# Kernel tuning notes

Hardware: AMD Instinct MI355X
Metric: run time of the kernel (lower is better)

Reference implementation:

```python
import jax, jax.numpy as jnp
import numpy as np

N = 2          # batch (upsample scale for sample i is i+1, shapes chosen so no crop occurs)
C = 512        # channels for both branches
TH = TW = 256  # target H,W taken from pts_feats[0]
IMG_SIZES = [128, 64, 32, 16, 8]  # 5-level FPN
BN_EPS = 1e-5


def setup_inputs() -> dict:
    key = jax.random.key(0)
    ks = jax.random.split(key, 24)
    inp = {}
    for l, s in enumerate(IMG_SIZES):
        inp[f'img_feat{l}'] = jax.random.normal(ks[l], (N, C, s, s), jnp.float32)
    inp['pts_feat0'] = jax.random.normal(ks[5], (N, C, TH, TW), jnp.float32)
    # 1x1 conv + BN params (eval-mode BN with running stats)
    inp['img_w'] = jax.random.normal(ks[6], (C, C), jnp.float32) * 0.02
    inp['img_b'] = jax.random.normal(ks[7], (C,), jnp.float32) * 0.02
    inp['img_gamma'] = jnp.ones((C,), jnp.float32)
    inp['img_beta'] = jnp.zeros((C,), jnp.float32)
    inp['img_mean'] = jnp.zeros((C,), jnp.float32)
    inp['img_var'] = jax.random.uniform(ks[8], (C,), jnp.float32, 0.5, 1.5)
    inp['pts_w'] = jax.random.normal(ks[9], (C, C), jnp.float32) * 0.02
    inp['pts_b'] = jax.random.normal(ks[10], (C,), jnp.float32) * 0.02
    inp['pts_gamma'] = jnp.ones((C,), jnp.float32)
    inp['pts_beta'] = jnp.zeros((C,), jnp.float32)
    inp['pts_mean'] = jnp.zeros((C,), jnp.float32)
    inp['pts_var'] = jax.random.uniform(ks[11], (C,), jnp.float32, 0.5, 1.5)
    return inp


def _obtain_mlvl(feats, th, tw):
    # Faithful to original: per-sample loop (scale_factor depends on batch index,
    # so each sample has a different static upsampled shape -> Python loop over N=2).
    n = feats[0].shape[0]
    outs = []
    for i in range(n):
        acc = None
        for lvl, f in enumerate(feats):
            x = f[i]  # [C, h, w]
            if lvl > 0:
                s = i + 1  # nearest upsample by batch-index+1 (as in source)
                x = jnp.repeat(jnp.repeat(x, s, axis=1), s, axis=2)
            dh = th - x.shape[1]
            dw = tw - x.shape[2]
            x = jnp.pad(x, ((0, 0), (dh // 2, dh - dh // 2), (dw // 2, dw - dw // 2)), mode='edge')
            acc = x if acc is None else acc + x
        outs.append(acc)
    return jnp.stack(outs, 0)  # [N, C, th, tw]


def _conv_bn_relu(x, w, b, gamma, beta, mean, var):
    # 1x1 conv == channel contraction, then eval-mode BN, then ReLU
    y = jnp.einsum('nchw,oc->nohw', x, w) + b[None, :, None, None]
    scale = gamma / jnp.sqrt(var + BN_EPS)
    y = (y - mean[None, :, None, None]) * scale[None, :, None, None] + beta[None, :, None, None]
    return jax.nn.relu(y)


def reference(img_feat0, img_feat1, img_feat2, img_feat3, img_feat4, pts_feat0,
              img_w, img_b, img_gamma, img_beta, img_mean, img_var,
              pts_w, pts_b, pts_gamma, pts_beta, pts_mean, pts_var):
    th, tw = pts_feat0.shape[2], pts_feat0.shape[3]
    pts_m = _obtain_mlvl([pts_feat0], th, tw)  # pts_levels=1
    pts_pre = _conv_bn_relu(pts_m, pts_w, pts_b, pts_gamma, pts_beta, pts_mean, pts_var)
    img_m = _obtain_mlvl([img_feat0, img_feat1, img_feat2, img_feat3, img_feat4], th, tw)
    img_pre = _conv_bn_relu(img_m, img_w, img_b, img_gamma, img_beta, img_mean, img_var)
    # dropout is identity in eval mode (deterministic reference)
    return jnp.concatenate((img_pre, pts_pre), axis=1)  # [N, 2C, th, tw]
```

## Files before the change

### kernel.cpp

```cpp
#include <hip/hip_runtime.h>

typedef unsigned short u16;
typedef __attribute__((ext_vector_type(8))) short s8frag;
typedef __attribute__((ext_vector_type(4))) float f32x4;

#define GLOAD16(gp, lp)                                                        \
  __builtin_amdgcn_global_load_lds(                                            \
      (const __attribute__((address_space(1))) void*)(gp),                     \
      (__attribute__((address_space(3))) void*)(lp), 16, 0, 0)

__device__ __forceinline__ u16 f2bf(float x) {
  unsigned int u = __float_as_uint(x);
  unsigned int r = (u + 0x7fffu + ((u >> 16) & 1u)) >> 16;
  return (u16)r;
}

__global__ __launch_bounds__(256) void prep_w(
    const float* __restrict__ wi, const float* __restrict__ bi,
    const float* __restrict__ gi, const float* __restrict__ bei,
    const float* __restrict__ mi, const float* __restrict__ vi,
    const float* __restrict__ wp, const float* __restrict__ bp,
    const float* __restrict__ gp, const float* __restrict__ bep,
    const float* __restrict__ mp, const float* __restrict__ vp,
    u16* __restrict__ wout_i, float* __restrict__ bias_i,
    u16* __restrict__ wout_p, float* __restrict__ bias_p) {
  int gidx = blockIdx.x * 256 + threadIdx.x;
  int branch = gidx >> 18;
  int idx = gidx & ((1 << 18) - 1);
  int o = idx >> 9, c = idx & 511;
  const float* w = branch ? wp : wi;
  const float* b = branch ? bp : bi;
  const float* g = branch ? gp : gi;
  const float* be = branch ? bep : bei;
  const float* mn = branch ? mp : mi;
  const float* vr = branch ? vp : vi;
  u16* wo = branch ? wout_p : wout_i;
  float* bo = branch ? bias_p : bias_i;
  float scale = g[o] * rsqrtf(vr[o] + 1e-5f);
  wo[idx] = f2bf(w[idx] * scale);
  if (c == 0) bo[o] = scale * (b[o] - mn[o]) + be[o];
}

__global__ __launch_bounds__(256) void build_b(
    const float* __restrict__ f0, const float* __restrict__ f1,
    const float* __restrict__ f2, const float* __restrict__ f3,
    const float* __restrict__ f4, const float* __restrict__ pts,
    u16* __restrict__ Bimg, u16* __restrict__ Bpts) {
  __shared__ float tile[64][65];
  int t = threadIdx.x;
  int wblk = blockIdx.x;
  int h = blockIdx.y;
  int z = blockIdx.z;
  bool is_img = z < 16;
  int zz = is_img ? z : z - 16;
  int n = zz >> 3;
  int cblk = zz & 7;
  int cbase = cblk * 64;

  if (is_img) {
    int wl = t & 63, w = wblk * 64 + wl;
    const float* feats[5] = {f0, f1, f2, f3, f4};
    const int S[5] = {128, 64, 32, 16, 8};
    int off[5];
#pragma unroll
    for (int l = 0; l < 5; ++l) {
      int s = S[l];
      int scale = (n == 1 && l > 0) ? 2 : 1;
      int u = s * scale, pad = (256 - u) >> 1;
      int ih = h - pad; ih = ih < 0 ? 0 : (ih > u - 1 ? u - 1 : ih); ih /= scale;
      int iw = w - pad; iw = iw < 0 ? 0 : (iw > u - 1 ? u - 1 : iw); iw /= scale;
      off[l] = ih * s + iw;
    }
    for (int cs = 0; cs < 16; ++cs) {
      int cl = cs * 4 + (t >> 6);
      int c = cbase + cl;
      float acc = 0.f;
#pragma unroll
      for (int l = 0; l < 5; ++l) {
        int s = S[l];
        acc += feats[l][(long)(n * 512 + c) * s * s + off[l]];
      }
      tile[cl][wl] = acc;
    }
  } else {
    int wq = t & 15;
    int cl0 = t >> 4;
#pragma unroll
    for (int j = 0; j < 4; ++j) {
      int cl = cl0 + j * 16;
      int c = cbase + cl;
      float4 v = *(const float4*)&pts[((long)(n * 512 + c) * 256 + h) * 256 +
                                      wblk * 64 + wq * 4];
      tile[cl][wq * 4 + 0] = v.x;
      tile[cl][wq * 4 + 1] = v.y;
      tile[cl][wq * 4 + 2] = v.z;
      tile[cl][wq * 4 + 3] = v.w;
    }
  }
  __syncthreads();

  u16* dst = is_img ? Bimg : Bpts;
  long hwb = (long)h * 256 + wblk * 64;
#pragma unroll
  for (int half = 0; half < 2; ++half) {
    int c0 = (t & 7) * 8;
    int wl2 = half * 32 + (t >> 3);
    u16 p[8];
#pragma unroll
    for (int j = 0; j < 8; ++j) p[j] = f2bf(tile[c0 + j][wl2]);
    long di = ((long)n * 65536 + hwb + wl2) * 512 + cbase + c0;
    *(uint4*)(dst + di) = *(const uint4*)p;
  }
}

__global__ __launch_bounds__(256) void gemm_fused(
    const u16* __restrict__ Aimg, const u16* __restrict__ Apts,
    const u16* __restrict__ Bimg, const u16* __restrict__ Bpts,
    const float* __restrict__ biasImg, const float* __restrict__ biasPts,
    float* __restrict__ out) {
  int br = blockIdx.z;
  const u16* A = br ? Apts : Aimg;
  const u16* B = br ? Bpts : Bimg;
  const float* bias = br ? biasPts : biasImg;

  int s = blockIdx.x;
  int w = (s & 7) * 512 + (s >> 3);
  int rt = w & 3;
  int ct = w >> 2;
  int n = ct >> 9;
  int colbase = (ct & 511) * 128;
  const u16* Bn = B + ((long)n * 65536) * 512;

  __shared__ u16 As[3][128 * 32];
  __shared__ u16 Bs[3][128 * 32];

  int t = threadIdx.x;
  int wave = t >> 6, lane = t & 63;
  int wr = wave >> 1, wc = wave & 1;
  int lrow = lane & 15;
  int q = lane >> 4;

  f32x4 acc[4][4] = {};

#define STAGE_A(buf, kk)                                                      \
  {                                                                           \
    _Pragma("unroll") for (int i = 0; i < 2; ++i) {                           \
      int slot = t + i * 256;                                                 \
      int row = slot >> 2, kp = slot & 3;                                     \
      int sw = (row >> 1) & 3;                                                \
      GLOAD16(A + ((long)(rt * 128 + row) * 512 + (kk) + ((kp ^ sw) * 8)),    \
              &As[buf][slot * 8]);                                            \
    }                                                                         \
  }
#define STAGE_B(buf, kk)                                                      \
  {                                                                           \
    _Pragma("unroll") for (int i = 0; i < 2; ++i) {                           \
      int slot = t + i * 256;                                                 \
      int row = slot >> 2, kp = slot & 3;                                     \
      int sw = (row >> 1) & 3;                                                \
      GLOAD16(Bn + ((long)(colbase + row) * 512 + (kk) + ((kp ^ sw) * 8)),    \
              &Bs[buf][slot * 8]);                                            \
    }                                                                         \
  }

  STAGE_A(0, 0);
  STAGE_B(0, 0);
  STAGE_A(1, 32);
  STAGE_B(1, 32);
  asm volatile("s_waitcnt vmcnt(4)" ::: "memory");
  __builtin_amdgcn_s_barrier();

  for (int kt = 0; kt < 16; ++kt) {
    int cur = kt % 3;
    int nb = (kt + 2) % 3;
    s8frag a0, a1, b[4];
    {
      int r0 = wr * 64 + 0 * 16 + lrow;
      a0 = *(const s8frag*)&As[cur][r0 * 32 + ((q ^ ((r0 >> 1) & 3)) * 8)];
      int r1 = wr * 64 + 1 * 16 + lrow;
      a1 = *(const s8frag*)&As[cur][r1 * 32 + ((q ^ ((r1 >> 1) & 3)) * 8)];
#pragma unroll
      for (int nn = 0; nn < 4; ++nn) {
        int r = wc * 64 + nn * 16 + lrow;
        b[nn] = *(const s8frag*)&Bs[cur][r * 32 + ((q ^ ((r >> 1) & 3)) * 8)];
      }
    }
    if (kt < 14) STAGE_A(nb, (kt + 2) * 32);
    __builtin_amdgcn_s_setprio(1);
#pragma unroll
    for (int nn = 0; nn < 4; ++nn)
      acc[0][nn] = __builtin_amdgcn_mfma_f32_16x16x32_bf16(a0, b[nn], acc[0][nn], 0, 0, 0);
#pragma unroll
    for (int nn = 0; nn < 4; ++nn)
      acc[1][nn] = __builtin_amdgcn_mfma_f32_16x16x32_bf16(a1, b[nn], acc[1][nn], 0, 0, 0);
    __builtin_amdgcn_s_setprio(0);
    __builtin_amdgcn_s_barrier();

    s8frag a2, a3;
    {
      int r2 = wr * 64 + 2 * 16 + lrow;
      a2 = *(const s8frag*)&As[cur][r2 * 32 + ((q ^ ((r2 >> 1) & 3)) * 8)];
      int r3 = wr * 64 + 3 * 16 + lrow;
      a3 = *(const s8frag*)&As[cur][r3 * 32 + ((q ^ ((r3 >> 1) & 3)) * 8)];
    }
    if (kt < 14) STAGE_B(nb, (kt + 2) * 32);
    __builtin_amdgcn_s_setprio(1);
#pragma unroll
    for (int nn = 0; nn < 4; ++nn)
      acc[2][nn] = __builtin_amdgcn_mfma_f32_16x16x32_bf16(a2, b[nn], acc[2][nn], 0, 0, 0);
#pragma unroll
    for (int nn = 0; nn < 4; ++nn)
      acc[3][nn] = __builtin_amdgcn_mfma_f32_16x16x32_bf16(a3, b[nn], acc[3][nn], 0, 0, 0);
    __builtin_amdgcn_s_setprio(0);
    if (kt < 15) {
      if (kt < 14)
        asm volatile("s_waitcnt vmcnt(4)" ::: "memory");
      else
        asm volatile("s_waitcnt vmcnt(0)" ::: "memory");
      __builtin_amdgcn_s_barrier();
    }
  }
#undef STAGE_A
#undef STAGE_B

  long outbase = ((long)n * 1024 + br * 512) * 65536;
#pragma unroll
  for (int m = 0; m < 4; ++m) {
    int o0 = rt * 128 + wr * 64 + m * 16 + (lane >> 4) * 4;
#pragma unroll
    for (int nn = 0; nn < 4; ++nn) {
      int hw = colbase + wc * 64 + nn * 16 + (lane & 15);
#pragma unroll
      for (int j = 0; j < 4; ++j) {
        int o = o0 + j;
        float v = acc[m][nn][j] + bias[o];
        v = v > 0.f ? v : 0.f;
        out[outbase + (long)o * 65536 + hw] = v;
      }
    }
  }
}

extern "C" void kernel_launch(void* const* d_in, const int* in_sizes, int n_in,
                              void* d_out, int out_size, void* d_ws,
                              size_t ws_size, hipStream_t stream) {
  (void)in_sizes; (void)n_in; (void)out_size; (void)ws_size;
  const float* f0 = (const float*)d_in[0];
  const float* f1 = (const float*)d_in[1];
  const float* f2 = (const float*)d_in[2];
  const float* f3 = (const float*)d_in[3];
  const float* f4 = (const float*)d_in[4];
  const float* pts = (const float*)d_in[5];
  const float* img_w = (const float*)d_in[6];
  const float* img_b = (const float*)d_in[7];
  const float* img_gamma = (const float*)d_in[8];
  const float* img_beta = (const float*)d_in[9];
  const float* img_mean = (const float*)d_in[10];
  const float* img_var = (const float*)d_in[11];
  const float* pts_w = (const float*)d_in[12];
  const float* pts_b = (const float*)d_in[13];
  const float* pts_gamma = (const float*)d_in[14];
  const float* pts_beta = (const float*)d_in[15];
  const float* pts_mean = (const float*)d_in[16];
  const float* pts_var = (const float*)d_in[17];

  char* ws = (char*)d_ws;
  u16* wA_img = (u16*)ws;
  u16* wA_pts = wA_img + 512 * 512;
  float* bias_img = (float*)(ws + (1u << 20));
  float* bias_pts = bias_img + 512;
  u16* Bimg = (u16*)(ws + (2u << 20));
  u16* Bpts = Bimg + (size_t)2 * 65536 * 512;

  prep_w<<<2048, 256, 0, stream>>>(img_w, img_b, img_gamma, img_beta, img_mean,
                                   img_var, pts_w, pts_b, pts_gamma, pts_beta,
                                   pts_mean, pts_var, wA_img, bias_img, wA_pts,
                                   bias_pts);
  build_b<<<dim3(4, 256, 32), 256, 0, stream>>>(f0, f1, f2, f3, f4, pts, Bimg,
                                                Bpts);
  gemm_fused<<<dim3(4096, 1, 2), 256, 0, stream>>>(
      wA_img, wA_pts, Bimg, Bpts, bias_img, bias_pts, (float*)d_out);
}
```

Before: 485.1 us.

## Load GEMM fragments directly from global memory, dropping LDS staging and barriers

Replaces the triple-buffered LDS pipeline (global_load_lds plus swizzled LDS reads and barriers) with direct per-wave global loads of the MFMA operand fragments, register double-buffered across K steps. It also sets launch bounds to request three blocks per CU. The aim is to remove the LDS traffic and synchronisation overhead, at the cost of redundant global/L2 reads: each A and B fragment row is now fetched by two waves instead of once per block. The 16-byte per-lane loads stride 1 KB between rows, so coalescing is poorer than before.

```diff
diff --git a/kernel.cpp b/kernel.cpp
--- a/kernel.cpp
+++ b/kernel.cpp
@@ -3,11 +3,6 @@
 typedef unsigned short u16;
 typedef __attribute__((ext_vector_type(8))) short s8frag;
 typedef __attribute__((ext_vector_type(4))) float f32x4;
-
-#define GLOAD16(gp, lp)                                                        \
-  __builtin_amdgcn_global_load_lds(                                            \
-      (const __attribute__((address_space(1))) void*)(gp),                     \
-      (__attribute__((address_space(3))) void*)(lp), 16, 0, 0)
 
 __device__ __forceinline__ u16 f2bf(float x) {
   unsigned int u = __float_as_uint(x);
@@ -113,7 +108,7 @@
   }
 }
 
-__global__ __launch_bounds__(256) void gemm_fused(
+__global__ __launch_bounds__(256, 3) void gemm_direct(
     const u16* __restrict__ Aimg, const u16* __restrict__ Apts,
     const u16* __restrict__ Bimg, const u16* __restrict__ Bpts,
     const float* __restrict__ biasImg, const float* __restrict__ biasPts,
@@ -131,97 +126,46 @@
   int colbase = (ct & 511) * 128;
   const u16* Bn = B + ((long)n * 65536) * 512;
 
-  __shared__ u16 As[3][128 * 32];
-  __shared__ u16 Bs[3][128 * 32];
-
   int t = threadIdx.x;
   int wave = t >> 6, lane = t & 63;
   int wr = wave >> 1, wc = wave & 1;
   int lrow = lane & 15;
   int q = lane >> 4;
 
+  const u16* pa = A + ((long)(rt * 128 + wr * 64 + lrow) * 512) + q * 8;
+  const u16* pb = Bn + ((long)(colbase + wc * 64 + lrow) * 512) + q * 8;
+
   f32x4 acc[4][4] = {};
-
-#define STAGE_A(buf, kk)                                                      \
+  s8frag aX[4], bX[4], aY[4], bY[4];
+
+#define LOADF(av, bv, kt_)                                                    \
   {                                                                           \
-    _Pragma("unroll") for (int i = 0; i < 2; ++i) {                           \
-      int slot = t + i * 256;                                                 \
-      int row = slot >> 2, kp = slot & 3;                                     \
-      int sw = (row >> 1) & 3;                                                \
-      GLOAD16(A + ((long)(rt * 128 + row) * 512 + (kk) + ((kp ^ sw) * 8)),    \
-              &As[buf][slot * 8]);                                            \
-    }                                                                         \
-  }
-#define STAGE_B(buf, kk)                                                      \
+    _Pragma("unroll") for (int m = 0; m < 4; ++m)                             \
+        av[m] = *(const s8frag*)(pa + (long)m * 8192 + (kt_) * 32);           \
+    _Pragma("unroll") for (int nn = 0; nn < 4; ++nn)                          \
+        bv[nn] = *(const s8frag*)(pb + (long)nn * 8192 + (kt_) * 32);         \
+  }
+#define MF(av, bv)                                                            \
   {                                                                           \
-    _Pragma("unroll") for (int i = 0; i < 2; ++i) {                           \
-      int slot = t + i * 256;                                                 \
-      int row = slot >> 2, kp = slot & 3;                                     \
-      int sw = (row >> 1) & 3;                                                \
-      GLOAD16(Bn + ((long)(colbase + row) * 512 + (kk) + ((kp ^ sw) * 8)),    \
-              &Bs[buf][slot * 8]);                                            \
-    }                                                                         \
-  }
-
-  STAGE_A(0, 0);
-  STAGE_B(0, 0);
-  STAGE_A(1, 32);
-  STAGE_B(1, 32);
-  asm volatile("s_waitcnt vmcnt(4)" ::: "memory");
-  __builtin_amdgcn_s_barrier();
-
-  for (int kt = 0; kt < 16; ++kt) {
-    int cur = kt % 3;
-    int nb = (kt + 2) % 3;
-    s8frag a0, a1, b[4];
-    {
-      int r0 = wr * 64 + 0 * 16 + lrow;
-      a0 = *(const s8frag*)&As[cur][r0 * 32 + ((q ^ ((r0 >> 1) & 3)) * 8)];
-      int r1 = wr * 64 + 1 * 16 + lrow;
-      a1 = *(const s8frag*)&As[cur][r1 * 32 + ((q ^ ((r1 >> 1) & 3)) * 8)];
-#pragma unroll
-      for (int nn = 0; nn < 4; ++nn) {
-        int r = wc * 64 + nn * 16 + lrow;
-        b[nn] = *(const s8frag*)&Bs[cur][r * 32 + ((q ^ ((r >> 1) & 3)) * 8)];
-      }
-    }
-    if (kt < 14) STAGE_A(nb, (kt + 2) * 32);
-    __builtin_amdgcn_s_setprio(1);
-#pragma unroll
-    for (int nn = 0; nn < 4; ++nn)
-      acc[0][nn] = __builtin_amdgcn_mfma_f32_16x16x32_bf16(a0, b[nn], acc[0][nn], 0, 0, 0);
-#pragma unroll
-    for (int nn = 0; nn < 4; ++nn)
-      acc[1][nn] = __builtin_amdgcn_mfma_f32_16x16x32_bf16(a1, b[nn], acc[1][nn], 0, 0, 0);
-    __builtin_amdgcn_s_setprio(0);
-    __builtin_amdgcn_s_barrier();
-
-    s8frag a2, a3;
-    {
-      int r2 = wr * 64 + 2 * 16 + lrow;
-      a2 = *(const s8frag*)&As[cur][r2 * 32 + ((q ^ ((r2 >> 1) & 3)) * 8)];
-      int r3 = wr * 64 + 3 * 16 + lrow;
-      a3 = *(const s8frag*)&As[cur][r3 * 32 + ((q ^ ((r3 >> 1) & 3)) * 8)];
-    }
-    if (kt < 14) STAGE_B(nb, (kt + 2) * 32);
-    __builtin_amdgcn_s_setprio(1);
-#pragma unroll
-    for (int nn = 0; nn < 4; ++nn)
-      acc[2][nn] = __builtin_amdgcn_mfma_f32_16x16x32_bf16(a2, b[nn], acc[2][nn], 0, 0, 0);
-#pragma unroll
-    for (int nn = 0; nn < 4; ++nn)
-      acc[3][nn] = __builtin_amdgcn_mfma_f32_16x16x32_bf16(a3, b[nn], acc[3][nn], 0, 0, 0);
-    __builtin_amdgcn_s_setprio(0);
-    if (kt < 15) {
-      if (kt < 14)
-        asm volatile("s_waitcnt vmcnt(4)" ::: "memory");
-      else
-        asm volatile("s_waitcnt vmcnt(0)" ::: "memory");
-      __builtin_amdgcn_s_barrier();
-    }
-  }
-#undef STAGE_A
-#undef STAGE_B
+    _Pragma("unroll") for (int m = 0; m < 4; ++m)                             \
+        _Pragma("unroll") for (int nn = 0; nn < 4; ++nn)                      \
+            acc[m][nn] = __builtin_amdgcn_mfma_f32_16x16x32_bf16(             \
+                av[m], bv[nn], acc[m][nn], 0, 0, 0);                          \
+  }
+
+  LOADF(aX, bX, 0);
+#pragma unroll 1
+  for (int kt2 = 0; kt2 < 7; ++kt2) {
+    LOADF(aY, bY, 2 * kt2 + 1);
+    MF(aX, bX);
+    LOADF(aX, bX, 2 * kt2 + 2);
+    MF(aY, bY);
+  }
+  LOADF(aY, bY, 15);
+  MF(aX, bX);
+  MF(aY, bY);
+#undef LOADF
+#undef MF
 
   long outbase = ((long)n * 1024 + br * 512) * 65536;
 #pragma unroll
@@ -278,6 +222,6 @@
                                    bias_pts);
   build_b<<<dim3(4, 256, 32), 256, 0, stream>>>(f0, f1, f2, f3, f4, pts, Bimg,
                                                 Bpts);
-  gemm_fused<<<dim3(4096, 1, 2), 256, 0, stream>>>(
+  gemm_direct<<<dim3(4096, 1, 2), 256, 0, stream>>>(
       wA_img, wA_pts, Bimg, Bpts, bias_img, bias_pts, (float*)d_out);
 }
```

New measurement: 763.0 us. +57.3%, slower.

## Enlarge GEMM tile to 256x256 with 512 threads and 4-stage pipeline

Applied to the files above, without the earlier changes.

Doubles the GEMM block tile from 128x128 to 256x256, using 8 waves per block with a 128x64 sub-tile each and 4 LDS buffers with three stages in flight. This raises arithmetic intensity per LDS and global load and cuts the block count by four. In exchange it uses 128 KB of LDS and 128 accumulator registers per lane, which forces one block per CU and risks lower occupancy and less latency hiding.

```diff
diff --git a/kernel.cpp b/kernel.cpp
--- a/kernel.cpp
+++ b/kernel.cpp
@@ -113,7 +113,7 @@
   }
 }
 
-__global__ __launch_bounds__(256) void gemm_fused(
+__global__ __launch_bounds__(512, 1) void gemm_fused(
     const u16* __restrict__ Aimg, const u16* __restrict__ Apts,
     const u16* __restrict__ Bimg, const u16* __restrict__ Bpts,
     const float* __restrict__ biasImg, const float* __restrict__ biasPts,
@@ -124,96 +124,97 @@
   const float* bias = br ? biasPts : biasImg;
 
   int s = blockIdx.x;
-  int w = (s & 7) * 512 + (s >> 3);
-  int rt = w & 3;
-  int ct = w >> 2;
-  int n = ct >> 9;
-  int colbase = (ct & 511) * 128;
+  int w = (s & 7) * 128 + (s >> 3);
+  int rt = w & 1;
+  int ct = w >> 1;
+  int n = ct >> 8;
+  int colbase = (ct & 255) * 256;
   const u16* Bn = B + ((long)n * 65536) * 512;
 
-  __shared__ u16 As[3][128 * 32];
-  __shared__ u16 Bs[3][128 * 32];
+  __shared__ u16 As[4][256 * 32];
+  __shared__ u16 Bs[4][256 * 32];
 
   int t = threadIdx.x;
   int wave = t >> 6, lane = t & 63;
-  int wr = wave >> 1, wc = wave & 1;
+  int wr = wave >> 2, wc = wave & 3;
   int lrow = lane & 15;
   int q = lane >> 4;
 
-  f32x4 acc[4][4] = {};
-
-#define STAGE_A(buf, kk)                                                      \
+  f32x4 acc[8][4] = {};
+
+#define STAGE_A(buf, kt_)                                                     \
   {                                                                           \
+    int kk_ = (kt_) * 32;                                                     \
     _Pragma("unroll") for (int i = 0; i < 2; ++i) {                           \
-      int slot = t + i * 256;                                                 \
+      int slot = t + i * 512;                                                 \
       int row = slot >> 2, kp = slot & 3;                                     \
       int sw = (row >> 1) & 3;                                                \
-      GLOAD16(A + ((long)(rt * 128 + row) * 512 + (kk) + ((kp ^ sw) * 8)),    \
+      GLOAD16(A + ((long)(rt * 256 + row) * 512 + kk_ + ((kp ^ sw) * 8)),     \
               &As[buf][slot * 8]);                                            \
     }                                                                         \
   }
-#define STAGE_B(buf, kk)                                                      \
+#define STAGE_B(buf, kt_)                                                     \
   {                                                                           \
+    int kk_ = (kt_) * 32;                                                     \
     _Pragma("unroll") for (int i = 0; i < 2; ++i) {                           \
-      int slot = t + i * 256;                                                 \
+      int slot = t + i * 512;                                                 \
       int row = slot >> 2, kp = slot & 3;                                     \
       int sw = (row >> 1) & 3;                                                \
-      GLOAD16(Bn + ((long)(colbase + row) * 512 + (kk) + ((kp ^ sw) * 8)),    \
+      GLOAD16(Bn + ((long)(colbase + row) * 512 + kk_ + ((kp ^ sw) * 8)),     \
               &Bs[buf][slot * 8]);                                            \
     }                                                                         \
   }
 
-  STAGE_A(0, 0);
-  STAGE_B(0, 0);
-  STAGE_A(1, 32);
-  STAGE_B(1, 32);
-  asm volatile("s_waitcnt vmcnt(4)" ::: "memory");
+  STAGE_A(0, 0); STAGE_B(0, 0);
+  STAGE_A(1, 1); STAGE_B(1, 1);
+  STAGE_A(2, 2); STAGE_B(2, 2);
+  asm volatile("s_waitcnt vmcnt(8)" ::: "memory");
   __builtin_amdgcn_s_barrier();
 
+#pragma unroll 1
   for (int kt = 0; kt < 16; ++kt) {
-    int cur = kt % 3;
-    int nb = (kt + 2) % 3;
-    s8frag a0, a1, b[4];
-    {
-      int r0 = wr * 64 + 0 * 16 + lrow;
-      a0 = *(const s8frag*)&As[cur][r0 * 32 + ((q ^ ((r0 >> 1) & 3)) * 8)];
-      int r1 = wr * 64 + 1 * 16 + lrow;
-      a1 = *(const s8frag*)&As[cur][r1 * 32 + ((q ^ ((r1 >> 1) & 3)) * 8)];
-#pragma unroll
-      for (int nn = 0; nn < 4; ++nn) {
-        int r = wc * 64 + nn * 16 + lrow;
-        b[nn] = *(const s8frag*)&Bs[cur][r * 32 + ((q ^ ((r >> 1) & 3)) * 8)];
-      }
-    }
-    if (kt < 14) STAGE_A(nb, (kt + 2) * 32);
+    int cur = kt & 3;
+    int nb = (kt + 3) & 3;
+    s8frag a[8], b[4];
+#pragma unroll
+    for (int m = 0; m < 4; ++m) {
+      int r = wr * 128 + m * 16 + lrow;
+      a[m] = *(const s8frag*)&As[cur][r * 32 + ((q ^ ((r >> 1) & 3)) * 8)];
+    }
+#pragma unroll
+    for (int nn = 0; nn < 4; ++nn) {
+      int r = wc * 64 + nn * 16 + lrow;
+      b[nn] = *(const s8frag*)&Bs[cur][r * 32 + ((q ^ ((r >> 1) & 3)) * 8)];
+    }
+    if (kt < 13) STAGE_A(nb, kt + 3);
     __builtin_amdgcn_s_setprio(1);
 #pragma unroll
-    for (int nn = 0; nn < 4; ++nn)
-      acc[0][nn] = __builtin_amdgcn_mfma_f32_16x16x32_bf16(a0, b[nn], acc[0][nn], 0, 0, 0);
-#pragma unroll
-    for (int nn = 0; nn < 4; ++nn)
-      acc[1][nn] = __builtin_amdgcn_mfma_f32_16x16x32_bf16(a1, b[nn], acc[1][nn], 0, 0, 0);
+    for (int m = 0; m < 4; ++m)
+#pragma unroll
+      for (int nn = 0; nn < 4; ++nn)
+        acc[m][nn] =
+            __builtin_amdgcn_mfma_f32_16x16x32_bf16(a[m], b[nn], acc[m][nn], 0, 0, 0);
     __builtin_amdgcn_s_setprio(0);
     __builtin_amdgcn_s_barrier();
 
-    s8frag a2, a3;
-    {
-      int r2 = wr * 64 + 2 * 16 + lrow;
-      a2 = *(const s8frag*)&As[cur][r2 * 32 + ((q ^ ((r2 >> 1) & 3)) * 8)];
-      int r3 = wr * 64 + 3 * 16 + lrow;
-      a3 = *(const s8frag*)&As[cur][r3 * 32 + ((q ^ ((r3 >> 1) & 3)) * 8)];
-    }
-    if (kt < 14) STAGE_B(nb, (kt + 2) * 32);
+#pragma unroll
+    for (int m = 4; m < 8; ++m) {
+      int r = wr * 128 + m * 16 + lrow;
+      a[m] = *(const s8frag*)&As[cur][r * 32 + ((q ^ ((r >> 1) & 3)) * 8)];
+    }
+    if (kt < 13) STAGE_B(nb, kt + 3);
     __builtin_amdgcn_s_setprio(1);
 #pragma unroll
-    for (int nn = 0; nn < 4; ++nn)
-      acc[2][nn] = __builtin_amdgcn_mfma_f32_16x16x32_bf16(a2, b[nn], acc[2][nn], 0, 0, 0);
-#pragma unroll
-    for (int nn = 0; nn < 4; ++nn)
-      acc[3][nn] = __builtin_amdgcn_mfma_f32_16x16x32_bf16(a3, b[nn], acc[3][nn], 0, 0, 0);
+    for (int m = 4; m < 8; ++m)
+#pragma unroll
+      for (int nn = 0; nn < 4; ++nn)
+        acc[m][nn] =
+            __builtin_amdgcn_mfma_f32_16x16x32_bf16(a[m], b[nn], acc[m][nn], 0, 0, 0);
     __builtin_amdgcn_s_setprio(0);
     if (kt < 15) {
-      if (kt < 14)
+      if (kt <= 12)
+        asm volatile("s_waitcnt vmcnt(8)" ::: "memory");
+      else if (kt == 13)
         asm volatile("s_waitcnt vmcnt(4)" ::: "memory");
       else
         asm volatile("s_waitcnt vmcnt(0)" ::: "memory");
@@ -225,11 +226,11 @@
 
   long outbase = ((long)n * 1024 + br * 512) * 65536;
 #pragma unroll
-  for (int m = 0; m < 4; ++m) {
-    int o0 = rt * 128 + wr * 64 + m * 16 + (lane >> 4) * 4;
+  for (int m = 0; m < 8; ++m) {
+    int o0 = rt * 256 + wr * 128 + m * 16 + q * 4;
 #pragma unroll
     for (int nn = 0; nn < 4; ++nn) {
-      int hw = colbase + wc * 64 + nn * 16 + (lane & 15);
+      int hw = colbase + wc * 64 + nn * 16 + lrow;
 #pragma unroll
       for (int j = 0; j < 4; ++j) {
         int o = o0 + j;
@@ -278,6 +279,6 @@
                                    bias_pts);
   build_b<<<dim3(4, 256, 32), 256, 0, stream>>>(f0, f1, f2, f3, f4, pts, Bimg,
                                                 Bpts);
-  gemm_fused<<<dim3(4096, 1, 2), 256, 0, stream>>>(
+  gemm_fused<<<dim3(1024, 1, 2), 512, 0, stream>>>(
       wA_img, wA_pts, Bimg, Bpts, bias_img, bias_pts, (float*)d_out);
 }
```

Result: no change. 480.9 us (-0.9%).

## Switch GEMM to double-buffered 64-wide K tiles with fewer barriers

Applied to the files above, without the earlier changes.

The fused 1x1-conv GEMM drops its three-stage pipeline of 32-wide K slices and uses two LDS buffers holding 64-wide K slices. The XOR swizzle is widened to 8 chunks to match. Each iteration loads all A/B fragments, prefetches the next slice, runs 32 MFMAs, and syncs once, so there are 8 barriers instead of about 31. Launch bounds now request 2 blocks per CU, and LDS use per block grows from 48KB to 64KB. The trade-off is less prefetch depth, with a full vmcnt(0) wait every iteration, and more register pressure from holding 16 fragments.

```diff
diff --git a/kernel.cpp b/kernel.cpp
--- a/kernel.cpp
+++ b/kernel.cpp
@@ -113,7 +113,7 @@
   }
 }
 
-__global__ __launch_bounds__(256) void gemm_fused(
+__global__ __launch_bounds__(256, 2) void gemm_fused(
     const u16* __restrict__ Aimg, const u16* __restrict__ Apts,
     const u16* __restrict__ Bimg, const u16* __restrict__ Bpts,
     const float* __restrict__ biasImg, const float* __restrict__ biasPts,
@@ -131,8 +131,8 @@
   int colbase = (ct & 511) * 128;
   const u16* Bn = B + ((long)n * 65536) * 512;
 
-  __shared__ u16 As[3][128 * 32];
-  __shared__ u16 Bs[3][128 * 32];
+  __shared__ u16 As[2][128 * 64];
+  __shared__ u16 Bs[2][128 * 64];
 
   int t = threadIdx.x;
   int wave = t >> 6, lane = t & 63;
@@ -142,81 +142,66 @@
 
   f32x4 acc[4][4] = {};
 
-#define STAGE_A(buf, kk)                                                      \
+#define STAGE_A(buf, kt_)                                                     \
   {                                                                           \
-    _Pragma("unroll") for (int i = 0; i < 2; ++i) {                           \
+    int kk_ = (kt_) * 64;                                                     \
+    _Pragma("unroll") for (int i = 0; i < 4; ++i) {                           \
       int slot = t + i * 256;                                                 \
-      int row = slot >> 2, kp = slot & 3;                                     \
-      int sw = (row >> 1) & 3;                                                \
-      GLOAD16(A + ((long)(rt * 128 + row) * 512 + (kk) + ((kp ^ sw) * 8)),    \
+      int row = slot >> 3, kp = slot & 7;                                     \
+      GLOAD16(A + ((long)(rt * 128 + row) * 512 + kk_ + ((kp ^ (row & 7)) * 8)), \
               &As[buf][slot * 8]);                                            \
     }                                                                         \
   }
-#define STAGE_B(buf, kk)                                                      \
+#define STAGE_B(buf, kt_)                                                     \
   {                                                                           \
-    _Pragma("unroll") for (int i = 0; i < 2; ++i) {                           \
+    int kk_ = (kt_) * 64;                                                     \
+    _Pragma("unroll") for (int i = 0; i < 4; ++i) {                           \
       int slot = t + i * 256;                                                 \
-      int row = slot >> 2, kp = slot & 3;                                     \
-      int sw = (row >> 1) & 3;                                                \
-      GLOAD16(Bn + ((long)(colbase + row) * 512 + (kk) + ((kp ^ sw) * 8)),    \
+      int row = slot >> 3, kp = slot & 7;                                     \
+      GLOAD16(Bn + ((long)(colbase + row) * 512 + kk_ + ((kp ^ (row & 7)) * 8)), \
               &Bs[buf][slot * 8]);                                            \
     }                                                                         \
   }
 
   STAGE_A(0, 0);
   STAGE_B(0, 0);
-  STAGE_A(1, 32);
-  STAGE_B(1, 32);
-  asm volatile("s_waitcnt vmcnt(4)" ::: "memory");
+  asm volatile("s_waitcnt vmcnt(0)" ::: "memory");
   __builtin_amdgcn_s_barrier();
 
-  for (int kt = 0; kt < 16; ++kt) {
-    int cur = kt % 3;
-    int nb = (kt + 2) % 3;
-    s8frag a0, a1, b[4];
-    {
-      int r0 = wr * 64 + 0 * 16 + lrow;
-      a0 = *(const s8frag*)&As[cur][r0 * 32 + ((q ^ ((r0 >> 1) & 3)) * 8)];
-      int r1 = wr * 64 + 1 * 16 + lrow;
-      a1 = *(const s8frag*)&As[cur][r1 * 32 + ((q ^ ((r1 >> 1) & 3)) * 8)];
+#pragma unroll 1
+  for (int kt = 0; kt < 8; ++kt) {
+    int cur = kt & 1;
+    s8frag a[2][4], b[2][4];
+#pragma unroll
+    for (int sl = 0; sl < 2; ++sl) {
+      int c = sl * 4 + q;
+#pragma unroll
+      for (int m = 0; m < 4; ++m) {
+        int r = wr * 64 + m * 16 + lrow;
+        a[sl][m] = *(const s8frag*)&As[cur][r * 64 + ((c ^ (r & 7)) * 8)];
+      }
 #pragma unroll
       for (int nn = 0; nn < 4; ++nn) {
         int r = wc * 64 + nn * 16 + lrow;
-        b[nn] = *(const s8frag*)&Bs[cur][r * 32 + ((q ^ ((r >> 1) & 3)) * 8)];
-      }
-    }
-    if (kt < 14) STAGE_A(nb, (kt + 2) * 32);
+        b[sl][nn] = *(const s8frag*)&Bs[cur][r * 64 + ((c ^ (r & 7)) * 8)];
+      }
+    }
+    if (kt < 7) {
+      STAGE_A(cur ^ 1, kt + 1);
+      STAGE_B(cur ^ 1, kt + 1);
+    }
     __builtin_amdgcn_s_setprio(1);
 #pragma unroll
-    for (int nn = 0; nn < 4; ++nn)
-      acc[0][nn] = __builtin_amdgcn_mfma_f32_16x16x32_bf16(a0, b[nn], acc[0][nn], 0, 0, 0);
-#pragma unroll
-    for (int nn = 0; nn < 4; ++nn)
-      acc[1][nn] = __builtin_amdgcn_mfma_f32_16x16x32_bf16(a1, b[nn], acc[1][nn], 0, 0, 0);
+    for (int sl = 0; sl < 2; ++sl)
+#pragma unroll
+      for (int m = 0; m < 4; ++m)
+#pragma unroll
+        for (int nn = 0; nn < 4; ++nn)
+          acc[m][nn] = __builtin_amdgcn_mfma_f32_16x16x32_bf16(
+              a[sl][m], b[sl][nn], acc[m][nn], 0, 0, 0);
     __builtin_amdgcn_s_setprio(0);
-    __builtin_amdgcn_s_barrier();
-
-    s8frag a2, a3;
-    {
-      int r2 = wr * 64 + 2 * 16 + lrow;
-      a2 = *(const s8frag*)&As[cur][r2 * 32 + ((q ^ ((r2 >> 1) & 3)) * 8)];
-      int r3 = wr * 64 + 3 * 16 + lrow;
-      a3 = *(const s8frag*)&As[cur][r3 * 32 + ((q ^ ((r3 >> 1) & 3)) * 8)];
-    }
-    if (kt < 14) STAGE_B(nb, (kt + 2) * 32);
-    __builtin_amdgcn_s_setprio(1);
-#pragma unroll
-    for (int nn = 0; nn < 4; ++nn)
-      acc[2][nn] = __builtin_amdgcn_mfma_f32_16x16x32_bf16(a2, b[nn], acc[2][nn], 0, 0, 0);
-#pragma unroll
-    for (int nn = 0; nn < 4; ++nn)
-      acc[3][nn] = __builtin_amdgcn_mfma_f32_16x16x32_bf16(a3, b[nn], acc[3][nn], 0, 0, 0);
-    __builtin_amdgcn_s_setprio(0);
-    if (kt < 15) {
-      if (kt < 14)
-        asm volatile("s_waitcnt vmcnt(4)" ::: "memory");
-      else
-        asm volatile("s_waitcnt vmcnt(0)" ::: "memory");
+    if (kt < 7) {
+      asm volatile("s_waitcnt vmcnt(0)" ::: "memory");
       __builtin_amdgcn_s_barrier();
     }
   }
@@ -226,10 +211,10 @@
   long outbase = ((long)n * 1024 + br * 512) * 65536;
 #pragma unroll
   for (int m = 0; m < 4; ++m) {
-    int o0 = rt * 128 + wr * 64 + m * 16 + (lane >> 4) * 4;
+    int o0 = rt * 128 + wr * 64 + m * 16 + q * 4;
 #pragma unroll
     for (int nn = 0; nn < 4; ++nn) {
-      int hw = colbase + wc * 64 + nn * 16 + (lane & 15);
+      int hw = colbase + wc * 64 + nn * 16 + lrow;
 #pragma unroll
       for (int j = 0; j < 4; ++j) {
         int o = o0 + j;
```

Result: slower. 506.6 us (+4.4%).
